# Kernel tuning notes

Hardware: AMD Instinct MI355X
Metric: run time of the kernel (lower is better)

## Reference

```python
import jax, jax.numpy as jnp
import numpy as np

N = 2097152
RES = 512
N_LEVELS = 6  # 512,256,128,64,32,16 (stop at LIGHT_MIN_RES=16)
MIN_ROUGHNESS = 0.08
MAX_ROUGHNESS = 0.5


def _dot(a, b):
    return jnp.sum(a * b, axis=-1, keepdims=True)


def _safe_normalize(x):
    return x / jnp.sqrt(jnp.clip(_dot(x, x), 1e-20, None))


def _reflect(x, n):
    return 2.0 * _dot(x, n) * n - x


def _rgb_to_srgb(x):
    return jnp.where(x <= 0.0031308, 12.92 * x,
                     1.055 * jnp.power(jnp.maximum(x, 0.0031308), 1.0 / 2.4) - 0.055)


def _cube_face_uv(d):
    # OpenGL / nvdiffrast cube-map convention (inverse of util.cube_to_dir)
    x, y, z = d[..., 0], d[..., 1], d[..., 2]
    ax, ay, az = jnp.abs(x), jnp.abs(y), jnp.abs(z)
    is_x = (ax >= ay) & (ax >= az)
    is_y = (~is_x) & (ay >= az)
    face = jnp.where(is_x, jnp.where(x > 0, 0, 1),
           jnp.where(is_y, jnp.where(y > 0, 2, 3),
                           jnp.where(z > 0, 4, 5)))
    ma = jnp.maximum(jnp.where(is_x, ax, jnp.where(is_y, ay, az)), 1e-20)
    u = jnp.where(is_x, jnp.where(x > 0, -z, z),
        jnp.where(is_y, x, jnp.where(z > 0, x, -x)))
    v = jnp.where(is_y, jnp.where(y > 0, z, -z), -y)
    return face, u / ma, v / ma


def _bilinear_gather(tex, face, fx, fy):
    # tex: [6,H,W,C]; face/fx/fy: [N]
    H, W = tex.shape[1], tex.shape[2]
    x0 = jnp.floor(fx); y0 = jnp.floor(fy)
    tx = (fx - x0)[:, None]; ty = (fy - y0)[:, None]
    x0i = jnp.clip(x0.astype(jnp.int32), 0, W - 1)
    x1i = jnp.clip(x0i + 1, 0, W - 1)
    y0i = jnp.clip(y0.astype(jnp.int32), 0, H - 1)
    y1i = jnp.clip(y0i + 1, 0, H - 1)
    c00 = tex[face, y0i, x0i]; c01 = tex[face, y0i, x1i]
    c10 = tex[face, y1i, x0i]; c11 = tex[face, y1i, x1i]
    return (c00 * (1 - tx) + c01 * tx) * (1 - ty) + (c10 * (1 - tx) + c11 * tx) * ty


def _sample_cubemap(tex, dirs):
    H, W = tex.shape[1], tex.shape[2]
    face, u, v = _cube_face_uv(dirs)
    return _bilinear_gather(tex, face, (u * 0.5 + 0.5) * W - 0.5, (v * 0.5 + 0.5) * H - 0.5)


def _sample_cubemap_mip(mips, dirs, level):
    # trilinear: bilinear in each of the two bracketing mip levels + lerp on level
    L = len(mips)
    samples = jnp.stack([_sample_cubemap(m, dirs) for m in mips], axis=0)  # [L,N,C]
    lvl = jnp.clip(level, 0.0, L - 1.0)
    l0 = jnp.floor(lvl).astype(jnp.int32)
    l1 = jnp.minimum(l0 + 1, L - 1)
    f = (lvl - l0.astype(lvl.dtype))[:, None]
    n = jnp.arange(dirs.shape[0])
    return samples[l0, n] * (1 - f) + samples[l1, n] * f


def _sample_lut(lut, uv):
    # lut: [H,W,C]; uv in [0,1], u -> width, v -> height, clamp boundary
    H, W = lut.shape[0], lut.shape[1]
    fx = uv[:, 0] * W - 0.5; fy = uv[:, 1] * H - 0.5
    x0 = jnp.floor(fx); y0 = jnp.floor(fy)
    tx = (fx - x0)[:, None]; ty = (fy - y0)[:, None]
    x0i = jnp.clip(x0.astype(jnp.int32), 0, W - 1); x1i = jnp.clip(x0i + 1, 0, W - 1)
    y0i = jnp.clip(y0.astype(jnp.int32), 0, H - 1); y1i = jnp.clip(y0i + 1, 0, H - 1)
    c00 = lut[y0i, x0i]; c01 = lut[y0i, x1i]; c10 = lut[y1i, x0i]; c11 = lut[y1i, x1i]
    return (c00 * (1 - tx) + c01 * tx) * (1 - ty) + (c10 * (1 - tx) + c11 * tx) * ty


def _get_mip(roughness, n_levels):
    lo = (jnp.clip(roughness, MIN_ROUGHNESS, MAX_ROUGHNESS) - MIN_ROUGHNESS) \
         / (MAX_ROUGHNESS - MIN_ROUGHNESS) * (n_levels - 2)
    hi = (jnp.clip(roughness, MAX_ROUGHNESS, 1.0) - MAX_ROUGHNESS) / (1.0 - MAX_ROUGHNESS) + n_levels - 2
    return jnp.where(roughness < MAX_ROUGHNESS, lo, hi)


def _shade(view_dir, normal, kd, ks, reflect_occ, diffuse_map, mips, fg_lut):
    roughness = ks[:, 1:2]
    metallic = ks[:, 2:3]
    spec_col = (1.0 - metallic) * 0.04 + kd * metallic
    diff_col = kd * (1.0 - metallic)
    reflvec = _safe_normalize(_reflect(view_dir, normal))
    diffuse = jnp.clip(_sample_cubemap(diffuse_map, normal), 0.0, None)
    shaded = diffuse * diff_col * (1.0 - ks[:, 0:1])
    NdotV = jnp.clip(_dot(view_dir, normal), 1e-4, None)
    fg = _sample_lut(fg_lut, jnp.concatenate([NdotV, roughness], axis=-1))
    miplevel = _get_mip(roughness[:, 0], len(mips))
    spec = jnp.clip(_sample_cubemap_mip(mips, reflvec, miplevel), 0.0, None)
    reflectance = spec_col * fg[:, 0:1] + fg[:, 1:2]
    shaded = shaded + spec * reflectance * (1.0 - reflect_occ)
    return _rgb_to_srgb(jnp.clip(shaded, 0.0, 1.0))


def setup_inputs() -> dict:
    key = jax.random.key(0)
    k = jax.random.split(key, 16)
    inp = {
        "view_dir": _safe_normalize(jax.random.normal(k[0], (N, 3), jnp.float32)),
        "normal": _safe_normalize(jax.random.normal(k[1], (N, 3), jnp.float32)),
        "kd": jax.random.uniform(k[2], (N, 3), jnp.float32),
        "ks": jax.random.uniform(k[3], (N, 3), jnp.float32),
        "reflect_occ": jax.random.uniform(k[4], (N, 1), jnp.float32),
    }
    # learned / prefiltered environment light parameters (from build_mips)
    inp["diffuse_map"] = jax.random.uniform(k[5], (6, 16, 16, 3), jnp.float32)
    res = RES
    for i in range(N_LEVELS):
        inp[f"spec{i}"] = jax.random.uniform(k[6 + i], (6, res, res, 3), jnp.float32)
        res //= 2
    inp["fg_lut"] = jax.random.uniform(k[12], (256, 256, 2), jnp.float32)
    return inp


def reference(view_dir, normal, kd, ks, reflect_occ, diffuse_map,
              spec0, spec1, spec2, spec3, spec4, spec5, fg_lut):
    mips = [spec0, spec1, spec2, spec3, spec4, spec5]
    return _shade(view_dir, normal, kd, ks, reflect_occ, diffuse_map, mips, fg_lut)
```

## Files before the change

kernel.cpp:

```cpp
#include <hip/hip_runtime.h>
#include <hip/hip_fp16.h>
#include <math.h>


typedef unsigned int u32;

__device__ __forceinline__ u32 enc9e5(float r, float g, float b) {
    r = fminf(fmaxf(r, 0.f), 65408.f);
    g = fminf(fmaxf(g, 0.f), 65408.f);
    b = fminf(fmaxf(b, 0.f), 65408.f);
    float maxc = fmaxf(r, fmaxf(g, b));
    int e = ((__float_as_int(maxc) >> 23) & 0xff) - 127;
    int exp_p = max(e + 16, 0);
    float rd = __int_as_float((151 - exp_p) << 23);
    int maxm = (int)(maxc * rd + 0.5f);
    if (maxm == 512) { exp_p += 1; rd *= 0.5f; }
    u32 rm = (u32)(r * rd + 0.5f);
    u32 gm = (u32)(g * rd + 0.5f);
    u32 bm = (u32)(b * rd + 0.5f);
    return rm | (gm << 9) | (bm << 18) | ((u32)exp_p << 27);
}

__device__ __forceinline__ void dec9e5_acc(u32 pk, float w, float& r, float& g, float& b) {
    float scale = __int_as_float((int)(((pk >> 27) & 31u) + 103u) << 23) * w;
    r += (float)(pk & 511u) * scale;
    g += (float)((pk >> 9) & 511u) * scale;
    b += (float)((pk >> 18) & 511u) * scale;
}

__device__ __forceinline__ void gather_q9(uint4 q, float tx, float ty,
                                          float& r, float& g, float& b) {
    float w00 = (1.f - tx) * (1.f - ty);
    float w01 = tx * (1.f - ty);
    float w10 = (1.f - tx) * ty;
    float w11 = tx * ty;
    r = 0.f; g = 0.f; b = 0.f;
    dec9e5_acc(q.x, w00, r, g, b);
    dec9e5_acc(q.y, w01, r, g, b);
    dec9e5_acc(q.z, w10, r, g, b);
    dec9e5_acc(q.w, w11, r, g, b);
}

__device__ __forceinline__ float srgb1(float x) {
    float p = 1.055f * __builtin_amdgcn_exp2f(
                  __builtin_amdgcn_logf(fmaxf(x, 0.0031308f)) * (1.0f / 2.4f)) - 0.055f;
    return (x <= 0.0031308f) ? (12.92f * x) : p;
}

__device__ __forceinline__ void cube_face_uv(float dx, float dy, float dz,
                                             int& face, float& u, float& v) {
    float ax = fabsf(dx), ay = fabsf(dy), az = fabsf(dz);
    bool is_x = (ax >= ay) && (ax >= az);
    bool is_y = (!is_x) && (ay >= az);
    face = is_x ? (dx > 0.f ? 0 : 1)
                : (is_y ? (dy > 0.f ? 2 : 3) : (dz > 0.f ? 4 : 5));
    float ma = fmaxf(is_x ? ax : (is_y ? ay : az), 1e-20f);
    float uu = is_x ? (dx > 0.f ? -dz : dz) : (is_y ? dx : (dz > 0.f ? dx : -dx));
    float vv = is_y ? (dy > 0.f ? dz : -dz) : -dy;
    float inv = __builtin_amdgcn_rcpf(ma);
    u = uu * inv;
    v = vv * inv;
}

#define SPEC_TOTAL 2096640
#define DIF_OFF    SPEC_TOTAL
#define LUT_OFF    (SPEC_TOTAL + 1536)
#define ALL_QUADS  (SPEC_TOTAL + 1536 + 65536)

__global__ __launch_bounds__(256)
void repack_all(const float* __restrict__ s0, const float* __restrict__ s1,
                const float* __restrict__ s2, const float* __restrict__ s3,
                const float* __restrict__ s4, const float* __restrict__ s5,
                const float* __restrict__ diffuse_map,
                const float2* __restrict__ lut,
                uint4* __restrict__ dst)
{
    int i = blockIdx.x * blockDim.x + threadIdx.x;
    if (i >= ALL_QUADS) return;

    if (i >= LUT_OFF) {
        int k = i - LUT_OFF;
        int y = k >> 8, x = k & 255;
        int x1 = min(x + 1, 255), y1 = min(y + 1, 255);
        float2 c00 = lut[(y << 8) + x],  c01 = lut[(y << 8) + x1];
        float2 c10 = lut[(y1 << 8) + x], c11 = lut[(y1 << 8) + x1];
        __half2 h00 = __floats2half2_rn(c00.x, c00.y);
        __half2 h01 = __floats2half2_rn(c01.x, c01.y);
        __half2 h10 = __floats2half2_rn(c10.x, c10.y);
        __half2 h11 = __floats2half2_rn(c11.x, c11.y);
        uint4 q;
        q.x = *reinterpret_cast<u32*>(&h00);
        q.y = *reinterpret_cast<u32*>(&h01);
        q.z = *reinterpret_cast<u32*>(&h10);
        q.w = *reinterpret_cast<u32*>(&h11);
        dst[i] = q;
        return;
    }

    const float* src;
    int lr, local;
    if (i >= DIF_OFF)       { src = diffuse_map; lr = 4; local = i - DIF_OFF; }
    else if (i < 1572864)   { src = s0; lr = 9; local = i; }
    else if (i < 1966080)   { src = s1; lr = 8; local = i - 1572864; }
    else if (i < 2064384)   { src = s2; lr = 7; local = i - 1966080; }
    else if (i < 2088960)   { src = s3; lr = 6; local = i - 2064384; }
    else if (i < 2095104)   { src = s4; lr = 5; local = i - 2088960; }
    else                    { src = s5; lr = 4; local = i - 2095104; }

    int W = 1 << lr;
    int face = local >> (2 * lr);
    int rem = local & (W * W - 1);
    int y = rem >> lr, x = rem & (W - 1);
    int x1 = min(x + 1, W - 1), y1 = min(y + 1, W - 1);
    int base = face << (2 * lr);
    int i00 = 3 * (base + (y << lr) + x);
    int i01 = 3 * (base + (y << lr) + x1);
    int i10 = 3 * (base + (y1 << lr) + x);
    int i11 = 3 * (base + (y1 << lr) + x1);
    uint4 q;
    q.x = enc9e5(src[i00], src[i00 + 1], src[i00 + 2]);
    q.y = enc9e5(src[i01], src[i01 + 1], src[i01 + 2]);
    q.z = enc9e5(src[i10], src[i10 + 1], src[i10 + 2]);
    q.w = enc9e5(src[i11], src[i11 + 1], src[i11 + 2]);
    dst[i] = q;
}

__global__ __launch_bounds__(256, 8)
void envlight_lds(const float* __restrict__ view_dir,
                  const float* __restrict__ normal,
                  const float* __restrict__ kd,
                  const float* __restrict__ ks,
                  const float* __restrict__ reflect_occ,
                  const uint4* __restrict__ q,
                  float* __restrict__ out, int n)
{
    __shared__ float s_in[3328];
    __shared__ float s_out[768];
    int tid = threadIdx.x;
    int base = blockIdx.x << 8;
    int nblk = min(256, n - base);

    if (nblk == 256) {
        const float4* v4 = (const float4*)(view_dir + 3 * base);
        const float4* n4 = (const float4*)(normal + 3 * base);
        const float4* k4 = (const float4*)(kd + 3 * base);
        const float4* q4 = (const float4*)(ks + 3 * base);
        const float4* o4 = (const float4*)(reflect_occ + base);
        float4* dst4 = (float4*)s_in;
        #pragma unroll
        for (int k = 0; k < 4; ++k) {
            int j = tid + (k << 8);
            if (j < 832) {
                const float4* src; int off;
                if (j < 192)      { src = v4; off = j; }
                else if (j < 384) { src = n4; off = j - 192; }
                else if (j < 576) { src = k4; off = j - 384; }
                else if (j < 768) { src = q4; off = j - 576; }
                else              { src = o4; off = j - 768; }
                dst4[j] = src[off];
            }
        }
    } else {
        for (int j = tid; j < nblk * 3; j += 256) {
            s_in[j]        = view_dir[3 * base + j];
            s_in[768 + j]  = normal[3 * base + j];
            s_in[1536 + j] = kd[3 * base + j];
            s_in[2304 + j] = ks[3 * base + j];
        }
        for (int j = tid; j < nblk; j += 256)
            s_in[3072 + j] = reflect_occ[base + j];
    }
    __syncthreads();

    if (tid < nblk) {
        float vx = s_in[3 * tid], vy = s_in[3 * tid + 1], vz = s_in[3 * tid + 2];
        float nx = s_in[768 + 3 * tid], ny = s_in[768 + 3 * tid + 1], nz = s_in[768 + 3 * tid + 2];
        float kdx = s_in[1536 + 3 * tid], kdy = s_in[1536 + 3 * tid + 1], kdz = s_in[1536 + 3 * tid + 2];
        float ks0 = s_in[2304 + 3 * tid], rough = s_in[2304 + 3 * tid + 1], metallic = s_in[2304 + 3 * tid + 2];
        float occ = s_in[3072 + tid];

        float vdotn = vx * nx + vy * ny + vz * nz;
        float rx = 2.f * vdotn * nx - vx;
        float ry = 2.f * vdotn * ny - vy;
        float rz = 2.f * vdotn * nz - vz;
        float rinv = __builtin_amdgcn_rsqf(fmaxf(rx * rx + ry * ry + rz * rz, 1e-20f));
        rx *= rinv; ry *= rinv; rz *= rinv;

        float dtx, dty; int dIdx;
        {
            int face; float u, v;
            cube_face_uv(nx, ny, nz, face, u, v);
            float fx = (u * 0.5f + 0.5f) * 16.f - 0.5f;
            float fy = (v * 0.5f + 0.5f) * 16.f - 0.5f;
            float x0f = floorf(fx), y0f = floorf(fy);
            dtx = fx - x0f; dty = fy - y0f;
            int x0 = min(max((int)x0f, 0), 15);
            int y0 = min(max((int)y0f, 0), 15);
            dIdx = (face << 8) + (y0 << 4) + x0;
        }

        float ltx, lty; int lutI;
        {
            float NdotV = fmaxf(vdotn, 1e-4f);
            float fx = NdotV * 256.f - 0.5f;
            float fy = rough * 256.f - 0.5f;
            float x0f = floorf(fx), y0f = floorf(fy);
            ltx = fx - x0f; lty = fy - y0f;
            int x0 = min(max((int)x0f, 0), 255);
            int y0 = min(max((int)y0f, 0), 255);
            lutI = (y0 << 8) + x0;
        }

        const float MINR = 0.08f, MAXR = 0.5f;
        float lo = (fminf(fmaxf(rough, MINR), MAXR) - MINR) * (4.0f / (MAXR - MINR));
        float hi = (fminf(fmaxf(rough, MAXR), 1.0f) - MAXR) * (1.0f / (1.0f - MAXR)) + 4.0f;
        float lvl = fminf(fmaxf((rough < MAXR) ? lo : hi, 0.f), 5.f);
        int l0 = min(max((int)floorf(lvl), 0), 5);
        int l1 = min(l0 + 1, 5);
        float fmip = lvl - (float)l0;

        float atx, aty, btx, bty; int aIdx, bIdx;
        {
            int face; float u, v;
            cube_face_uv(rx, ry, rz, face, u, v);
            int lrA = 9 - l0, lrB = 9 - l1;
            float RA = (float)(1 << lrA);
            float fxA = (u * 0.5f + 0.5f) * RA - 0.5f;
            float fyA = (v * 0.5f + 0.5f) * RA - 0.5f;
            float fxB = (l0 == l1) ? fxA : (fxA + 0.5f) * 0.5f - 0.5f;
            float fyB = (l0 == l1) ? fyA : (fyA + 0.5f) * 0.5f - 0.5f;

            float x0fA = floorf(fxA), y0fA = floorf(fyA);
            atx = fxA - x0fA; aty = fyA - y0fA;
            int WA = 1 << lrA;
            int x0A = min(max((int)x0fA, 0), WA - 1);
            int y0A = min(max((int)y0fA, 0), WA - 1);
            aIdx = (face << (2 * lrA)) + (y0A << lrA) + x0A;

            float x0fB = floorf(fxB), y0fB = floorf(fyB);
            btx = fxB - x0fB; bty = fyB - y0fB;
            int WB = 1 << lrB;
            int x0B = min(max((int)x0fB, 0), WB - 1);
            int y0B = min(max((int)y0fB, 0), WB - 1);
            bIdx = (face << (2 * lrB)) + (y0B << lrB) + x0B;
        }

        static const int OFF[6] = {0, 1572864, 1966080, 2064384, 2088960, 2095104};
        uint4 qA = (q + OFF[l0])[aIdx];
        uint4 qB = (q + OFF[l1])[bIdx];
        uint4 lq = (q + LUT_OFF)[lutI];
        uint4 dq = (q + DIF_OFF)[dIdx];

        float ar, ag, ab_, br, bg, bb;
        gather_q9(qA, atx, aty, ar, ag, ab_);
        gather_q9(qB, btx, bty, br, bg, bb);

        __half2 h00 = *reinterpret_cast<__half2*>(&lq.x);
        __half2 h01 = *reinterpret_cast<__half2*>(&lq.y);
        __half2 h10 = *reinterpret_cast<__half2*>(&lq.z);
        __half2 h11 = *reinterpret_cast<__half2*>(&lq.w);
        float2 c00 = __half22float2(h00), c01 = __half22float2(h01);
        float2 c10 = __half22float2(h10), c11 = __half22float2(h11);
        float lw00 = (1.f - ltx) * (1.f - lty);
        float lw01 = ltx * (1.f - lty);
        float lw10 = (1.f - ltx) * lty;
        float lw11 = ltx * lty;
        float fg0 = c00.x * lw00 + c01.x * lw01 + c10.x * lw10 + c11.x * lw11;
        float fg1 = c00.y * lw00 + c01.y * lw01 + c10.y * lw10 + c11.y * lw11;

        float dfr, dfg, dfb;
        gather_q9(dq, dtx, dty, dfr, dfg, dfb);
        dfr = fmaxf(dfr, 0.f); dfg = fmaxf(dfg, 0.f); dfb = fmaxf(dfb, 0.f);

        float spr = fmaxf(ar * (1.f - fmip) + br * fmip, 0.f);
        float spg = fmaxf(ag * (1.f - fmip) + bg * fmip, 0.f);
        float spb = fmaxf(ab_ * (1.f - fmip) + bb * fmip, 0.f);

        float m = metallic;
        float scx = (1.f - m) * 0.04f + kdx * m;
        float scy = (1.f - m) * 0.04f + kdy * m;
        float scz = (1.f - m) * 0.04f + kdz * m;
        float dcx = kdx * (1.f - m);
        float dcy = kdy * (1.f - m);
        float dcz = kdz * (1.f - m);

        float kds = 1.f - ks0;
        float om = 1.f - occ;
        float shx = dfr * dcx * kds + spr * (scx * fg0 + fg1) * om;
        float shy = dfg * dcy * kds + spg * (scy * fg0 + fg1) * om;
        float shz = dfb * dcz * kds + spb * (scz * fg0 + fg1) * om;

        s_out[3 * tid + 0] = srgb1(fminf(fmaxf(shx, 0.f), 1.f));
        s_out[3 * tid + 1] = srgb1(fminf(fmaxf(shy, 0.f), 1.f));
        s_out[3 * tid + 2] = srgb1(fminf(fmaxf(shz, 0.f), 1.f));
    }
    __syncthreads();

    if (nblk == 256) {
        if (tid < 192)
            ((float4*)(out + 3 * base))[tid] = ((const float4*)s_out)[tid];
    } else {
        for (int j = tid; j < nblk * 3; j += 256)
            out[3 * base + j] = s_out[j];
    }
}

__global__ __launch_bounds__(256)
void envlight_raw(const float* __restrict__ view_dir,
                  const float* __restrict__ normal,
                  const float* __restrict__ kd,
                  const float* __restrict__ ks,
                  const float* __restrict__ reflect_occ,
                  const float* __restrict__ diffuse_map,
                  const float* __restrict__ s0, const float* __restrict__ s1,
                  const float* __restrict__ s2, const float* __restrict__ s3,
                  const float* __restrict__ s4, const float* __restrict__ s5,
                  const float* __restrict__ fg_lut,
                  float* __restrict__ out, int n)
{
    int i = blockIdx.x * blockDim.x + threadIdx.x;
    if (i >= n) return;

    float vx = view_dir[3 * i], vy = view_dir[3 * i + 1], vz = view_dir[3 * i + 2];
    float nx = normal[3 * i],  ny = normal[3 * i + 1],  nz = normal[3 * i + 2];
    float kdx = kd[3 * i], kdy = kd[3 * i + 1], kdz = kd[3 * i + 2];
    float ks0 = ks[3 * i], rough = ks[3 * i + 1], metallic = ks[3 * i + 2];
    float occ = reflect_occ[i];

    float vdotn = vx * nx + vy * ny + vz * nz;
    float rx = 2.f * vdotn * nx - vx;
    float ry = 2.f * vdotn * ny - vy;
    float rz = 2.f * vdotn * nz - vz;
    float rinv = __builtin_amdgcn_rsqf(fmaxf(rx * rx + ry * ry + rz * rz, 1e-20f));
    rx *= rinv; ry *= rinv; rz *= rinv;

    const float* mips[6] = {s0, s1, s2, s3, s4, s5};

    const float MINR = 0.08f, MAXR = 0.5f;
    float lo = (fminf(fmaxf(rough, MINR), MAXR) - MINR) * (4.0f / (MAXR - MINR));
    float hi = (fminf(fmaxf(rough, MAXR), 1.0f) - MAXR) * (1.0f / (1.0f - MAXR)) + 4.0f;
    float lvl = fminf(fmaxf((rough < MAXR) ? lo : hi, 0.f), 5.f);
    int l0 = min(max((int)floorf(lvl), 0), 5);
    int l1 = min(l0 + 1, 5);
    float f = lvl - (float)l0;

    float acc[3][3];
    float dirs[3][3] = {{nx, ny, nz}, {rx, ry, rz}, {rx, ry, rz}};
    int lrs[3] = {4, 9 - l0, 9 - l1};
    const float* texs[3] = {diffuse_map, mips[l0], mips[l1]};
    for (int s = 0; s < 3; ++s) {
        int face; float u, v;
        cube_face_uv(dirs[s][0], dirs[s][1], dirs[s][2], face, u, v);
        int lr = lrs[s], W = 1 << lr;
        float fx = (u * 0.5f + 0.5f) * (float)W - 0.5f;
        float fy = (v * 0.5f + 0.5f) * (float)W - 0.5f;
        float x0f = floorf(fx), y0f = floorf(fy);
        float tx = fx - x0f, ty = fy - y0f;
        int x0 = min(max((int)x0f, 0), W - 1);
        int x1 = min(x0 + 1, W - 1);
        int y0 = min(max((int)y0f, 0), W - 1);
        int y1 = min(y0 + 1, W - 1);
        int base = face << (2 * lr);
        const float* t = texs[s];
        const float* p00 = t + 3 * (base + (y0 << lr) + x0);
        const float* p01 = t + 3 * (base + (y0 << lr) + x1);
        const float* p10 = t + 3 * (base + (y1 << lr) + x0);
        const float* p11 = t + 3 * (base + (y1 << lr) + x1);
        float w00 = (1.f - tx) * (1.f - ty), w01 = tx * (1.f - ty);
        float w10 = (1.f - tx) * ty, w11 = tx * ty;
        for (int c = 0; c < 3; ++c)
            acc[s][c] = p00[c] * w00 + p01[c] * w01 + p10[c] * w10 + p11[c] * w11;
    }

    float NdotV = fmaxf(vdotn, 1e-4f);
    float fx = NdotV * 256.f - 0.5f, fy = rough * 256.f - 0.5f;
    float x0f = floorf(fx), y0f = floorf(fy);
    float tx = fx - x0f, ty = fy - y0f;
    int x0 = min(max((int)x0f, 0), 255);
    int x1 = min(x0 + 1, 255);
    int y0 = min(max((int)y0f, 0), 255);
    int y1 = min(y0 + 1, 255);
    const float2* lut2 = (const float2*)fg_lut;
    float2 c00 = lut2[(y0 << 8) + x0], c01 = lut2[(y0 << 8) + x1];
    float2 c10 = lut2[(y1 << 8) + x0], c11 = lut2[(y1 << 8) + x1];
    float w00 = (1.f - tx) * (1.f - ty), w01 = tx * (1.f - ty);
    float w10 = (1.f - tx) * ty, w11 = tx * ty;
    float fg0 = c00.x * w00 + c01.x * w01 + c10.x * w10 + c11.x * w11;
    float fg1 = c00.y * w00 + c01.y * w01 + c10.y * w10 + c11.y * w11;

    float dfr = fmaxf(acc[0][0], 0.f), dfg = fmaxf(acc[0][1], 0.f), dfb = fmaxf(acc[0][2], 0.f);
    float spr = fmaxf(acc[1][0] * (1.f - f) + acc[2][0] * f, 0.f);
    float spg = fmaxf(acc[1][1] * (1.f - f) + acc[2][1] * f, 0.f);
    float spb = fmaxf(acc[1][2] * (1.f - f) + acc[2][2] * f, 0.f);

    float m = metallic;
    float scx = (1.f - m) * 0.04f + kdx * m;
    float scy = (1.f - m) * 0.04f + kdy * m;
    float scz = (1.f - m) * 0.04f + kdz * m;
    float kds = 1.f - ks0;
    float om = 1.f - occ;
    float shx = dfr * kdx * (1.f - m) * kds + spr * (scx * fg0 + fg1) * om;
    float shy = dfg * kdy * (1.f - m) * kds + spg * (scy * fg0 + fg1) * om;
    float shz = dfb * kdz * (1.f - m) * kds + spb * (scz * fg0 + fg1) * om;

    out[3 * i + 0] = srgb1(fminf(fmaxf(shx, 0.f), 1.f));
    out[3 * i + 1] = srgb1(fminf(fmaxf(shy, 0.f), 1.f));
    out[3 * i + 2] = srgb1(fminf(fmaxf(shz, 0.f), 1.f));
}

extern "C" void kernel_launch(void* const* d_in, const int* in_sizes, int n_in,
                              void* d_out, int out_size, void* d_ws, size_t ws_size,
                              hipStream_t stream) {
    const float* view_dir    = (const float*)d_in[0];
    const float* normal      = (const float*)d_in[1];
    const float* kd          = (const float*)d_in[2];
    const float* ks          = (const float*)d_in[3];
    const float* reflect_occ = (const float*)d_in[4];
    const float* diffuse_map = (const float*)d_in[5];
    const float* s0          = (const float*)d_in[6];
    const float* s1          = (const float*)d_in[7];
    const float* s2          = (const float*)d_in[8];
    const float* s3          = (const float*)d_in[9];
    const float* s4          = (const float*)d_in[10];
    const float* s5          = (const float*)d_in[11];
    const float* fg_lut      = (const float*)d_in[12];
    float* out = (float*)d_out;

    int n = in_sizes[0] / 3;
    int block = 256;
    int grid = (n + block - 1) / block;
    const size_t NEED_Q = (size_t)ALL_QUADS * 16;

    if (ws_size >= NEED_Q) {
        uint4* q = (uint4*)d_ws;
        repack_all<<<(ALL_QUADS + 255) / 256, 256, 0, stream>>>(
            s0, s1, s2, s3, s4, s5, diffuse_map, (const float2*)fg_lut, q);
        envlight_lds<<<grid, block, 0, stream>>>(
            view_dir, normal, kd, ks, reflect_occ, q, out, n);
    } else {
        envlight_raw<<<grid, block, 0, stream>>>(
            view_dir, normal, kd, ks, reflect_occ, diffuse_map,
            s0, s1, s2, s3, s4, s5, fg_lut, out, n);
    }
}
```

Before: 221.7 us.

## Tile texture repack through shared memory and process two points per thread

The repack kernel now loads each 16x16 texel tile plus a one-texel halo into shared memory once, encodes each texel a single time, and builds the 2x2 quads from LDS. Before, every texel was re-read and re-encoded four times. The shading kernel now handles 512 points per 256-thread block, two per thread, and issues all eight quad gathers before doing any finishing math, so more memory latency can overlap. In exchange it uses more registers (occupancy hint drops from 8 to 6), more LDS per block, and extra halo reads at tile edges.

After: 249.6 us. +12.5%, slower.

```diff
diff --git a/kernel.cpp b/kernel.cpp
--- a/kernel.cpp
+++ b/kernel.cpp
@@ -66,81 +66,217 @@
 #define DIF_OFF    SPEC_TOTAL
 #define LUT_OFF    (SPEC_TOTAL + 1536)
 #define ALL_QUADS  (SPEC_TOTAL + 1536 + 65536)
+#define N_TILES    8452
 
 __global__ __launch_bounds__(256)
-void repack_all(const float* __restrict__ s0, const float* __restrict__ s1,
-                const float* __restrict__ s2, const float* __restrict__ s3,
-                const float* __restrict__ s4, const float* __restrict__ s5,
-                const float* __restrict__ diffuse_map,
-                const float2* __restrict__ lut,
-                uint4* __restrict__ dst)
+void repack_tiled(const float* __restrict__ s0, const float* __restrict__ s1,
+                  const float* __restrict__ s2, const float* __restrict__ s3,
+                  const float* __restrict__ s4, const float* __restrict__ s5,
+                  const float* __restrict__ diffuse_map,
+                  const float2* __restrict__ lut,
+                  uint4* __restrict__ dst)
 {
-    int i = blockIdx.x * blockDim.x + threadIdx.x;
-    if (i >= ALL_QUADS) return;
-
-    if (i >= LUT_OFF) {
-        int k = i - LUT_OFF;
-        int y = k >> 8, x = k & 255;
-        int x1 = min(x + 1, 255), y1 = min(y + 1, 255);
-        float2 c00 = lut[(y << 8) + x],  c01 = lut[(y << 8) + x1];
-        float2 c10 = lut[(y1 << 8) + x], c11 = lut[(y1 << 8) + x1];
-        __half2 h00 = __floats2half2_rn(c00.x, c00.y);
-        __half2 h01 = __floats2half2_rn(c01.x, c01.y);
-        __half2 h10 = __floats2half2_rn(c10.x, c10.y);
-        __half2 h11 = __floats2half2_rn(c11.x, c11.y);
-        uint4 q;
-        q.x = *reinterpret_cast<u32*>(&h00);
-        q.y = *reinterpret_cast<u32*>(&h01);
-        q.z = *reinterpret_cast<u32*>(&h10);
-        q.w = *reinterpret_cast<u32*>(&h11);
-        dst[i] = q;
+    __shared__ u32 L[289];
+    int b = blockIdx.x;
+    int tid = threadIdx.x;
+
+    if (b >= 8196) {
+        int t = b - 8196;
+        int ty0 = (t >> 4) << 4;
+        int tx0 = (t & 15) << 4;
+        for (int e = tid; e < 289; e += 256) {
+            int ey = e / 17, ex = e - ey * 17;
+            int gy = min(ty0 + ey, 255), gx = min(tx0 + ex, 255);
+            float2 c = lut[(gy << 8) + gx];
+            __half2 h = __floats2half2_rn(c.x, c.y);
+            L[e] = *reinterpret_cast<u32*>(&h);
+        }
+        __syncthreads();
+        int qx = tid & 15, qy = tid >> 4;
+        uint4 qv;
+        qv.x = L[qy * 17 + qx];       qv.y = L[qy * 17 + qx + 1];
+        qv.z = L[(qy + 1) * 17 + qx]; qv.w = L[(qy + 1) * 17 + qx + 1];
+        dst[LUT_OFF + ((ty0 + qy) << 8) + tx0 + qx] = qv;
         return;
     }
 
-    const float* src;
-    int lr, local;
-    if (i >= DIF_OFF)       { src = diffuse_map; lr = 4; local = i - DIF_OFF; }
-    else if (i < 1572864)   { src = s0; lr = 9; local = i; }
-    else if (i < 1966080)   { src = s1; lr = 8; local = i - 1572864; }
-    else if (i < 2064384)   { src = s2; lr = 7; local = i - 1966080; }
-    else if (i < 2088960)   { src = s3; lr = 6; local = i - 2064384; }
-    else if (i < 2095104)   { src = s4; lr = 5; local = i - 2088960; }
-    else                    { src = s5; lr = 4; local = i - 2095104; }
+    const float* src; int lr, tbase, doff;
+    if      (b < 6144) { src = s0; lr = 9; tbase = 0;    doff = 0; }
+    else if (b < 7680) { src = s1; lr = 8; tbase = 6144; doff = 1572864; }
+    else if (b < 8064) { src = s2; lr = 7; tbase = 7680; doff = 1966080; }
+    else if (b < 8160) { src = s3; lr = 6; tbase = 8064; doff = 2064384; }
+    else if (b < 8184) { src = s4; lr = 5; tbase = 8160; doff = 2088960; }
+    else if (b < 8190) { src = s5; lr = 4; tbase = 8184; doff = 2095104; }
+    else               { src = diffuse_map; lr = 4; tbase = 8190; doff = DIF_OFF; }
 
     int W = 1 << lr;
-    int face = local >> (2 * lr);
-    int rem = local & (W * W - 1);
-    int y = rem >> lr, x = rem & (W - 1);
-    int x1 = min(x + 1, W - 1), y1 = min(y + 1, W - 1);
-    int base = face << (2 * lr);
-    int i00 = 3 * (base + (y << lr) + x);
-    int i01 = 3 * (base + (y << lr) + x1);
-    int i10 = 3 * (base + (y1 << lr) + x);
-    int i11 = 3 * (base + (y1 << lr) + x1);
-    uint4 q;
-    q.x = enc9e5(src[i00], src[i00 + 1], src[i00 + 2]);
-    q.y = enc9e5(src[i01], src[i01 + 1], src[i01 + 2]);
-    q.z = enc9e5(src[i10], src[i10 + 1], src[i10 + 2]);
-    q.w = enc9e5(src[i11], src[i11 + 1], src[i11 + 2]);
-    dst[i] = q;
-}
-
-__global__ __launch_bounds__(256, 8)
-void envlight_lds(const float* __restrict__ view_dir,
-                  const float* __restrict__ normal,
-                  const float* __restrict__ kd,
-                  const float* __restrict__ ks,
-                  const float* __restrict__ reflect_occ,
-                  const uint4* __restrict__ q,
-                  float* __restrict__ out, int n)
+    int lt = lr - 4;
+    int local = b - tbase;
+    int face = local >> (2 * lt);
+    int rem  = local & ((1 << (2 * lt)) - 1);
+    int ty0 = (rem >> lt) << 4;
+    int tx0 = (rem & ((1 << lt) - 1)) << 4;
+    int fbase = face << (2 * lr);
+
+    for (int e = tid; e < 289; e += 256) {
+        int ey = e / 17, ex = e - ey * 17;
+        int gy = min(ty0 + ey, W - 1), gx = min(tx0 + ex, W - 1);
+        int idx = 3 * (fbase + (gy << lr) + gx);
+        L[e] = enc9e5(src[idx], src[idx + 1], src[idx + 2]);
+    }
+    __syncthreads();
+    int qx = tid & 15, qy = tid >> 4;
+    uint4 qv;
+    qv.x = L[qy * 17 + qx];       qv.y = L[qy * 17 + qx + 1];
+    qv.z = L[(qy + 1) * 17 + qx]; qv.w = L[(qy + 1) * 17 + qx + 1];
+    dst[doff + fbase + ((ty0 + qy) << lr) + tx0 + qx] = qv;
+}
+
+
+struct PtA {
+    float kdx, kdy, kdz, ks0, met, occ;
+    float dtx, dty, ltx, lty, atx, aty, btx, bty, fmip;
+    int aI, bI, lI, dI;
+};
+
+__device__ __forceinline__ void prep_pt(const float* s, int t, PtA& p) {
+    float vx = s[3 * t],        vy = s[3 * t + 1],        vz = s[3 * t + 2];
+    float nx = s[1536 + 3 * t], ny = s[1536 + 3 * t + 1], nz = s[1536 + 3 * t + 2];
+    p.kdx = s[3072 + 3 * t]; p.kdy = s[3072 + 3 * t + 1]; p.kdz = s[3072 + 3 * t + 2];
+    p.ks0 = s[4608 + 3 * t];
+    float rough = s[4608 + 3 * t + 1];
+    p.met = s[4608 + 3 * t + 2];
+    p.occ = s[6144 + t];
+
+    float vdotn = vx * nx + vy * ny + vz * nz;
+    float rx = 2.f * vdotn * nx - vx;
+    float ry = 2.f * vdotn * ny - vy;
+    float rz = 2.f * vdotn * nz - vz;
+    float rinv = __builtin_amdgcn_rsqf(fmaxf(rx * rx + ry * ry + rz * rz, 1e-20f));
+    rx *= rinv; ry *= rinv; rz *= rinv;
+
+    {
+        int face; float u, v;
+        cube_face_uv(nx, ny, nz, face, u, v);
+        float fx = (u * 0.5f + 0.5f) * 16.f - 0.5f;
+        float fy = (v * 0.5f + 0.5f) * 16.f - 0.5f;
+        float x0f = floorf(fx), y0f = floorf(fy);
+        p.dtx = fx - x0f; p.dty = fy - y0f;
+        int x0 = min(max((int)x0f, 0), 15);
+        int y0 = min(max((int)y0f, 0), 15);
+        p.dI = DIF_OFF + (face << 8) + (y0 << 4) + x0;
+    }
+
+    {
+        float NdotV = fmaxf(vdotn, 1e-4f);
+        float fx = NdotV * 256.f - 0.5f;
+        float fy = rough * 256.f - 0.5f;
+        float x0f = floorf(fx), y0f = floorf(fy);
+        p.ltx = fx - x0f; p.lty = fy - y0f;
+        int x0 = min(max((int)x0f, 0), 255);
+        int y0 = min(max((int)y0f, 0), 255);
+        p.lI = LUT_OFF + (y0 << 8) + x0;
+    }
+
+    const float MINR = 0.08f, MAXR = 0.5f;
+    float lo = (fminf(fmaxf(rough, MINR), MAXR) - MINR) * (4.0f / (MAXR - MINR));
+    float hi = (fminf(fmaxf(rough, MAXR), 1.0f) - MAXR) * (1.0f / (1.0f - MAXR)) + 4.0f;
+    float lvl = fminf(fmaxf((rough < MAXR) ? lo : hi, 0.f), 5.f);
+    int l0 = min(max((int)floorf(lvl), 0), 5);
+    int l1 = min(l0 + 1, 5);
+    p.fmip = lvl - (float)l0;
+
+    {
+        int face; float u, v;
+        cube_face_uv(rx, ry, rz, face, u, v);
+        int lrA = 9 - l0, lrB = 9 - l1;
+        float RA = (float)(1 << lrA);
+        float fxA = (u * 0.5f + 0.5f) * RA - 0.5f;
+        float fyA = (v * 0.5f + 0.5f) * RA - 0.5f;
+        float fxB = (l0 == l1) ? fxA : (fxA + 0.5f) * 0.5f - 0.5f;
+        float fyB = (l0 == l1) ? fyA : (fyA + 0.5f) * 0.5f - 0.5f;
+
+        float x0fA = floorf(fxA), y0fA = floorf(fyA);
+        p.atx = fxA - x0fA; p.aty = fyA - y0fA;
+        int WA = 1 << lrA;
+        int x0A = min(max((int)x0fA, 0), WA - 1);
+        int y0A = min(max((int)y0fA, 0), WA - 1);
+        int aIdx = (face << (2 * lrA)) + (y0A << lrA) + x0A;
+
+        float x0fB = floorf(fxB), y0fB = floorf(fyB);
+        p.btx = fxB - x0fB; p.bty = fyB - y0fB;
+        int WB = 1 << lrB;
+        int x0B = min(max((int)x0fB, 0), WB - 1);
+        int y0B = min(max((int)y0fB, 0), WB - 1);
+        int bIdx = (face << (2 * lrB)) + (y0B << lrB) + x0B;
+
+        static const int OFF[6] = {0, 1572864, 1966080, 2064384, 2088960, 2095104};
+        p.aI = OFF[l0] + aIdx;
+        p.bI = OFF[l1] + bIdx;
+    }
+}
+
+__device__ __forceinline__ void finish_pt(const PtA& p, uint4 qA, uint4 qB,
+                                          uint4 lq, uint4 dq, float* o) {
+    float ar, ag, ab_, br, bg, bb;
+    gather_q9(qA, p.atx, p.aty, ar, ag, ab_);
+    gather_q9(qB, p.btx, p.bty, br, bg, bb);
+
+    __half2 h00 = *reinterpret_cast<__half2*>(&lq.x);
+    __half2 h01 = *reinterpret_cast<__half2*>(&lq.y);
+    __half2 h10 = *reinterpret_cast<__half2*>(&lq.z);
+    __half2 h11 = *reinterpret_cast<__half2*>(&lq.w);
+    float2 c00 = __half22float2(h00), c01 = __half22float2(h01);
+    float2 c10 = __half22float2(h10), c11 = __half22float2(h11);
+    float lw00 = (1.f - p.ltx) * (1.f - p.lty);
+    float lw01 = p.ltx * (1.f - p.lty);
+    float lw10 = (1.f - p.ltx) * p.lty;
+    float lw11 = p.ltx * p.lty;
+    float fg0 = c00.x * lw00 + c01.x * lw01 + c10.x * lw10 + c11.x * lw11;
+    float fg1 = c00.y * lw00 + c01.y * lw01 + c10.y * lw10 + c11.y * lw11;
+
+    float dfr, dfg, dfb;
+    gather_q9(dq, p.dtx, p.dty, dfr, dfg, dfb);
+    dfr = fmaxf(dfr, 0.f); dfg = fmaxf(dfg, 0.f); dfb = fmaxf(dfb, 0.f);
+
+    float spr = fmaxf(ar * (1.f - p.fmip) + br * p.fmip, 0.f);
+    float spg = fmaxf(ag * (1.f - p.fmip) + bg * p.fmip, 0.f);
+    float spb = fmaxf(ab_ * (1.f - p.fmip) + bb * p.fmip, 0.f);
+
+    float m = p.met;
+    float scx = (1.f - m) * 0.04f + p.kdx * m;
+    float scy = (1.f - m) * 0.04f + p.kdy * m;
+    float scz = (1.f - m) * 0.04f + p.kdz * m;
+    float dcx = p.kdx * (1.f - m);
+    float dcy = p.kdy * (1.f - m);
+    float dcz = p.kdz * (1.f - m);
+
+    float kds = 1.f - p.ks0;
+    float om = 1.f - p.occ;
+    float shx = dfr * dcx * kds + spr * (scx * fg0 + fg1) * om;
+    float shy = dfg * dcy * kds + spg * (scy * fg0 + fg1) * om;
+    float shz = dfb * dcz * kds + spb * (scz * fg0 + fg1) * om;
+
+    o[0] = srgb1(fminf(fmaxf(shx, 0.f), 1.f));
+    o[1] = srgb1(fminf(fmaxf(shy, 0.f), 1.f));
+    o[2] = srgb1(fminf(fmaxf(shz, 0.f), 1.f));
+}
+
+__global__ __launch_bounds__(256, 6)
+void envlight_lds2(const float* __restrict__ view_dir,
+                   const float* __restrict__ normal,
+                   const float* __restrict__ kd,
+                   const float* __restrict__ ks,
+                   const float* __restrict__ reflect_occ,
+                   const uint4* __restrict__ q,
+                   float* __restrict__ out, int n)
 {
-    __shared__ float s_in[3328];
-    __shared__ float s_out[768];
+    __shared__ float s_in[6656];
     int tid = threadIdx.x;
-    int base = blockIdx.x << 8;
-    int nblk = min(256, n - base);
-
-    if (nblk == 256) {
+    int base = blockIdx.x << 9;
+    int nblk = min(512, n - base);
+
+    if (nblk == 512) {
         const float4* v4 = (const float4*)(view_dir + 3 * base);
         const float4* n4 = (const float4*)(normal + 3 * base);
         const float4* k4 = (const float4*)(kd + 3 * base);
@@ -148,160 +284,72 @@
         const float4* o4 = (const float4*)(reflect_occ + base);
         float4* dst4 = (float4*)s_in;
         #pragma unroll
-        for (int k = 0; k < 4; ++k) {
+        for (int k = 0; k < 7; ++k) {
             int j = tid + (k << 8);
-            if (j < 832) {
+            if (j < 1664) {
                 const float4* src; int off;
-                if (j < 192)      { src = v4; off = j; }
-                else if (j < 384) { src = n4; off = j - 192; }
-                else if (j < 576) { src = k4; off = j - 384; }
-                else if (j < 768) { src = q4; off = j - 576; }
-                else              { src = o4; off = j - 768; }
+                if (j < 384)       { src = v4; off = j; }
+                else if (j < 768)  { src = n4; off = j - 384; }
+                else if (j < 1152) { src = k4; off = j - 768; }
+                else if (j < 1536) { src = q4; off = j - 1152; }
+                else               { src = o4; off = j - 1536; }
                 dst4[j] = src[off];
             }
         }
     } else {
         for (int j = tid; j < nblk * 3; j += 256) {
             s_in[j]        = view_dir[3 * base + j];
-            s_in[768 + j]  = normal[3 * base + j];
-            s_in[1536 + j] = kd[3 * base + j];
-            s_in[2304 + j] = ks[3 * base + j];
+            s_in[1536 + j] = normal[3 * base + j];
+            s_in[3072 + j] = kd[3 * base + j];
+            s_in[4608 + j] = ks[3 * base + j];
         }
         for (int j = tid; j < nblk; j += 256)
-            s_in[3072 + j] = reflect_occ[base + j];
+            s_in[6144 + j] = reflect_occ[base + j];
     }
     __syncthreads();
 
-    if (tid < nblk) {
-        float vx = s_in[3 * tid], vy = s_in[3 * tid + 1], vz = s_in[3 * tid + 2];
-        float nx = s_in[768 + 3 * tid], ny = s_in[768 + 3 * tid + 1], nz = s_in[768 + 3 * tid + 2];
-        float kdx = s_in[1536 + 3 * tid], kdy = s_in[1536 + 3 * tid + 1], kdz = s_in[1536 + 3 * tid + 2];
-        float ks0 = s_in[2304 + 3 * tid], rough = s_in[2304 + 3 * tid + 1], metallic = s_in[2304 + 3 * tid + 2];
-        float occ = s_in[3072 + tid];
-
-        float vdotn = vx * nx + vy * ny + vz * nz;
-        float rx = 2.f * vdotn * nx - vx;
-        float ry = 2.f * vdotn * ny - vy;
-        float rz = 2.f * vdotn * nz - vz;
-        float rinv = __builtin_amdgcn_rsqf(fmaxf(rx * rx + ry * ry + rz * rz, 1e-20f));
-        rx *= rinv; ry *= rinv; rz *= rinv;
-
-        float dtx, dty; int dIdx;
-        {
-            int face; float u, v;
-            cube_face_uv(nx, ny, nz, face, u, v);
-            float fx = (u * 0.5f + 0.5f) * 16.f - 0.5f;
-            float fy = (v * 0.5f + 0.5f) * 16.f - 0.5f;
-            float x0f = floorf(fx), y0f = floorf(fy);
-            dtx = fx - x0f; dty = fy - y0f;
-            int x0 = min(max((int)x0f, 0), 15);
-            int y0 = min(max((int)y0f, 0), 15);
-            dIdx = (face << 8) + (y0 << 4) + x0;
+    bool a0 = (tid < nblk);
+    bool a1 = (tid + 256 < nblk);
+
+    PtA p0, p1;
+    uint4 qA0, qB0, ql0, qd0, qA1, qB1, ql1, qd1;
+    float o0[3], o1[3];
+
+    if (a0) {
+        prep_pt(s_in, tid, p0);
+        qA0 = q[p0.aI]; qB0 = q[p0.bI]; ql0 = q[p0.lI]; qd0 = q[p0.dI];
+    }
+    if (a1) {
+        prep_pt(s_in, tid + 256, p1);
+        qA1 = q[p1.aI]; qB1 = q[p1.bI]; ql1 = q[p1.lI]; qd1 = q[p1.dI];
+    }
+    if (a0) finish_pt(p0, qA0, qB0, ql0, qd0, o0);
+    if (a1) finish_pt(p1, qA1, qB1, ql1, qd1, o1);
+
+    __syncthreads();
+
+    if (a0) {
+        s_in[3 * tid + 0] = o0[0];
+        s_in[3 * tid + 1] = o0[1];
+        s_in[3 * tid + 2] = o0[2];
+    }
+    if (a1) {
+        s_in[3 * (tid + 256) + 0] = o1[0];
+        s_in[3 * (tid + 256) + 1] = o1[1];
+        s_in[3 * (tid + 256) + 2] = o1[2];
+    }
+    __syncthreads();
+
+    if (nblk == 512) {
+        float4* ot4 = (float4*)(out + 3 * base);
+        #pragma unroll
+        for (int k = 0; k < 2; ++k) {
+            int j = tid + (k << 8);
+            if (j < 384) ot4[j] = ((const float4*)s_in)[j];
         }
-
-        float ltx, lty; int lutI;
-        {
-            float NdotV = fmaxf(vdotn, 1e-4f);
-            float fx = NdotV * 256.f - 0.5f;
-            float fy = rough * 256.f - 0.5f;
-            float x0f = floorf(fx), y0f = floorf(fy);
-            ltx = fx - x0f; lty = fy - y0f;
-            int x0 = min(max((int)x0f, 0), 255);
-            int y0 = min(max((int)y0f, 0), 255);
-            lutI = (y0 << 8) + x0;
-        }
-
-        const float MINR = 0.08f, MAXR = 0.5f;
-        float lo = (fminf(fmaxf(rough, MINR), MAXR) - MINR) * (4.0f / (MAXR - MINR));
-        float hi = (fminf(fmaxf(rough, MAXR), 1.0f) - MAXR) * (1.0f / (1.0f - MAXR)) + 4.0f;
-        float lvl = fminf(fmaxf((rough < MAXR) ? lo : hi, 0.f), 5.f);
-        int l0 = min(max((int)floorf(lvl), 0), 5);
-        int l1 = min(l0 + 1, 5);
-        float fmip = lvl - (float)l0;
-
-        float atx, aty, btx, bty; int aIdx, bIdx;
-        {
-            int face; float u, v;
-            cube_face_uv(rx, ry, rz, face, u, v);
-            int lrA = 9 - l0, lrB = 9 - l1;
-            float RA = (float)(1 << lrA);
-            float fxA = (u * 0.5f + 0.5f) * RA - 0.5f;
-            float fyA = (v * 0.5f + 0.5f) * RA - 0.5f;
-            float fxB = (l0 == l1) ? fxA : (fxA + 0.5f) * 0.5f - 0.5f;
-            float fyB = (l0 == l1) ? fyA : (fyA + 0.5f) * 0.5f - 0.5f;
-
-            float x0fA = floorf(fxA), y0fA = floorf(fyA);
-            atx = fxA - x0fA; aty = fyA - y0fA;
-            int WA = 1 << lrA;
-            int x0A = min(max((int)x0fA, 0), WA - 1);
-            int y0A = min(max((int)y0fA, 0), WA - 1);
-            aIdx = (face << (2 * lrA)) + (y0A << lrA) + x0A;
-
-            float x0fB = floorf(fxB), y0fB = floorf(fyB);
-            btx = fxB - x0fB; bty = fyB - y0fB;
-            int WB = 1 << lrB;
-            int x0B = min(max((int)x0fB, 0), WB - 1);
-            int y0B = min(max((int)y0fB, 0), WB - 1);
-            bIdx = (face << (2 * lrB)) + (y0B << lrB) + x0B;
-        }
-
-        static const int OFF[6] = {0, 1572864, 1966080, 2064384, 2088960, 2095104};
-        uint4 qA = (q + OFF[l0])[aIdx];
-        uint4 qB = (q + OFF[l1])[bIdx];
-        uint4 lq = (q + LUT_OFF)[lutI];
-        uint4 dq = (q + DIF_OFF)[dIdx];
-
-        float ar, ag, ab_, br, bg, bb;
-        gather_q9(qA, atx, aty, ar, ag, ab_);
-        gather_q9(qB, btx, bty, br, bg, bb);
-
-        __half2 h00 = *reinterpret_cast<__half2*>(&lq.x);
-        __half2 h01 = *reinterpret_cast<__half2*>(&lq.y);
-        __half2 h10 = *reinterpret_cast<__half2*>(&lq.z);
-        __half2 h11 = *reinterpret_cast<__half2*>(&lq.w);
-        float2 c00 = __half22float2(h00), c01 = __half22float2(h01);
-        float2 c10 = __half22float2(h10), c11 = __half22float2(h11);
-        float lw00 = (1.f - ltx) * (1.f - lty);
-        float lw01 = ltx * (1.f - lty);
-        float lw10 = (1.f - ltx) * lty;
-        float lw11 = ltx * lty;
-        float fg0 = c00.x * lw00 + c01.x * lw01 + c10.x * lw10 + c11.x * lw11;
-        float fg1 = c00.y * lw00 + c01.y * lw01 + c10.y * lw10 + c11.y * lw11;
-
-        float dfr, dfg, dfb;
-        gather_q9(dq, dtx, dty, dfr, dfg, dfb);
-        dfr = fmaxf(dfr, 0.f); dfg = fmaxf(dfg, 0.f); dfb = fmaxf(dfb, 0.f);
-
-        float spr = fmaxf(ar * (1.f - fmip) + br * fmip, 0.f);
-        float spg = fmaxf(ag * (1.f - fmip) + bg * fmip, 0.f);
-        float spb = fmaxf(ab_ * (1.f - fmip) + bb * fmip, 0.f);
-
-        float m = metallic;
-        float scx = (1.f - m) * 0.04f + kdx * m;
-        float scy = (1.f - m) * 0.04f + kdy * m;
-        float scz = (1.f - m) * 0.04f + kdz * m;
-        float dcx = kdx * (1.f - m);
-        float dcy = kdy * (1.f - m);
-        float dcz = kdz * (1.f - m);
-
-        float kds = 1.f - ks0;
-        float om = 1.f - occ;
-        float shx = dfr * dcx * kds + spr * (scx * fg0 + fg1) * om;
-        float shy = dfg * dcy * kds + spg * (scy * fg0 + fg1) * om;
-        float shz = dfb * dcz * kds + spb * (scz * fg0 + fg1) * om;
-
-        s_out[3 * tid + 0] = srgb1(fminf(fmaxf(shx, 0.f), 1.f));
-        s_out[3 * tid + 1] = srgb1(fminf(fmaxf(shy, 0.f), 1.f));
-        s_out[3 * tid + 2] = srgb1(fminf(fmaxf(shz, 0.f), 1.f));
-    }
-    __syncthreads();
-
-    if (nblk == 256) {
-        if (tid < 192)
-            ((float4*)(out + 3 * base))[tid] = ((const float4*)s_out)[tid];
     } else {
         for (int j = tid; j < nblk * 3; j += 256)
-            out[3 * base + j] = s_out[j];
+            out[3 * base + j] = s_in[j];
     }
 }
 
@@ -427,18 +475,18 @@
     float* out = (float*)d_out;
 
     int n = in_sizes[0] / 3;
-    int block = 256;
-    int grid = (n + block - 1) / block;
     const size_t NEED_Q = (size_t)ALL_QUADS * 16;
 
     if (ws_size >= NEED_Q) {
         uint4* q = (uint4*)d_ws;
-        repack_all<<<(ALL_QUADS + 255) / 256, 256, 0, stream>>>(
+        repack_tiled<<<N_TILES, 256, 0, stream>>>(
             s0, s1, s2, s3, s4, s5, diffuse_map, (const float2*)fg_lut, q);
-        envlight_lds<<<grid, block, 0, stream>>>(
+        int grid = (n + 511) / 512;
+        envlight_lds2<<<grid, 256, 0, stream>>>(
             view_dir, normal, kd, ks, reflect_occ, q, out, n);
     } else {
-        envlight_raw<<<grid, block, 0, stream>>>(
+        int grid = (n + 255) / 256;
+        envlight_raw<<<grid, 256, 0, stream>>>(
             view_dir, normal, kd, ks, reflect_occ, diffuse_map,
             s0, s1, s2, s3, s4, s5, fg_lut, out, n);
     }
```
